# Optimization experiments

Measured on AMD Instinct MI355X. Metric: run time of the kernel, lower is better.

The kernel has to match this reference:

```python
import jax, jax.numpy as jnp
import numpy as np

DIM = 1024
NUM_HEADS = 16
HEAD_DIM = DIM // NUM_HEADS
B, S = 2, 2048


def setup_inputs() -> dict:
    key = jax.random.key(0)
    ks = jax.random.split(key, 7)
    x = jax.random.normal(ks[0], (B, S, DIM), dtype=jnp.float32)
    cos = jax.random.uniform(ks[1], (S, HEAD_DIM // 2), dtype=jnp.float32)
    sin = jax.random.uniform(ks[2], (S, HEAD_DIM // 2), dtype=jnp.float32)
    scale = 1.0 / np.sqrt(DIM)
    Wq = jax.random.normal(ks[3], (DIM, DIM), dtype=jnp.float32) * scale
    Wk = jax.random.normal(ks[4], (DIM, DIM), dtype=jnp.float32) * scale
    Wv = jax.random.normal(ks[5], (DIM, DIM), dtype=jnp.float32) * scale
    Wo = jax.random.normal(ks[6], (DIM, DIM), dtype=jnp.float32) * scale
    return {"x": x, "cos": cos, "sin": sin, "Wq": Wq, "Wk": Wk, "Wv": Wv, "Wo": Wo}


def _apply_rope(t, c, s):
    # t: [B, S, H, hd]; c, s: [1, S, 1, hd] (already doubled)
    half = t.shape[-1] // 2
    t1, t2 = t[..., :half], t[..., half:]
    rot = jnp.concatenate([-t2, t1], axis=-1)
    return t * c + rot * s


def reference(x, cos, sin, Wq, Wk, Wv, Wo):
    Bs, Ss, D = x.shape
    H, hd = NUM_HEADS, HEAD_DIM
    q = (x @ Wq).reshape(Bs, Ss, H, hd)
    k = (x @ Wk).reshape(Bs, Ss, H, hd)
    v = (x @ Wv).reshape(Bs, Ss, H, hd)
    # repeat(1,1,1,2) in torch tiles cos as [cos, cos] along last dim
    c = jnp.concatenate([cos, cos], axis=-1)[None, :, None, :]
    s = jnp.concatenate([sin, sin], axis=-1)[None, :, None, :]
    q = _apply_rope(q, c, s)
    k = _apply_rope(k, c, s)
    # SDPA, non-causal, scale 1/sqrt(hd)
    scores = jnp.einsum("bqhd,bkhd->bhqk", q, k) / jnp.sqrt(jnp.float32(hd))
    attn = jax.nn.softmax(scores, axis=-1)
    out = jnp.einsum("bhqk,bkhd->bqhd", attn, v).reshape(Bs, Ss, D)
    return out @ Wo
```

## Files before the change

### kernel.cpp

```cpp
#include <hip/hip_runtime.h>

#define B_  2
#define S_  2048
#define D_  1024
#define H_  16
#define HD_ 64
#define M_  (B_*S_)

typedef __bf16 bf16x8 __attribute__((ext_vector_type(8)));
typedef float  f32x4  __attribute__((ext_vector_type(4)));
typedef float  f32x16 __attribute__((ext_vector_type(16)));
typedef unsigned short ushort_t;

static __device__ __forceinline__ ushort_t f2bf(float f) {
  __bf16 b = (__bf16)f;
  return __builtin_bit_cast(ushort_t, b);
}
static __device__ __forceinline__ float bf2f(ushort_t u) {
  return (float)__builtin_bit_cast(__bf16, u);
}

__global__ __launch_bounds__(256) void convert_x(const float* __restrict__ x,
                                                 ushort_t* __restrict__ xb) {
  size_t e = ((size_t)blockIdx.x * 256 + threadIdx.x) * 8;
  float4 a = *(const float4*)(x + e);
  float4 b = *(const float4*)(x + e + 4);
  uint4 pk;
  pk.x = (unsigned)f2bf(a.x) | ((unsigned)f2bf(a.y) << 16);
  pk.y = (unsigned)f2bf(a.z) | ((unsigned)f2bf(a.w) << 16);
  pk.z = (unsigned)f2bf(b.x) | ((unsigned)f2bf(b.y) << 16);
  pk.w = (unsigned)f2bf(b.z) | ((unsigned)f2bf(b.w) << 16);
  *(uint4*)(xb + e) = pk;
}

__global__ __launch_bounds__(256) void transpose_w(const float* __restrict__ Wq,
                                                   const float* __restrict__ Wk,
                                                   const float* __restrict__ Wv,
                                                   const float* __restrict__ Wo,
                                                   ushort_t* __restrict__ Wqkvt,
                                                   ushort_t* __restrict__ Wot) {
  __shared__ __bf16 T[64][72];
  const int z = blockIdx.z;
  const float* W = (z == 0) ? Wq : (z == 1) ? Wk : (z == 2) ? Wv : Wo;
  ushort_t* Wt = (z < 3) ? (Wqkvt + (size_t)z * 1048576) : Wot;
  const int k0 = blockIdx.y * 64, n0 = blockIdx.x * 64;
  const int t = threadIdx.x, r = t >> 2, c16 = (t & 3) * 16;
#pragma unroll
  for (int i = 0; i < 4; i++) {
    float4 v = *(const float4*)(W + (size_t)(k0 + r) * D_ + n0 + c16 + i * 4);
    T[r][c16 + i*4 + 0] = (__bf16)v.x;
    T[r][c16 + i*4 + 1] = (__bf16)v.y;
    T[r][c16 + i*4 + 2] = (__bf16)v.z;
    T[r][c16 + i*4 + 3] = (__bf16)v.w;
  }
  __syncthreads();
  ushort_t vals[16];
#pragma unroll
  for (int i = 0; i < 16; i++) vals[i] = __builtin_bit_cast(ushort_t, T[c16 + i][r]);
  ushort_t* dst = Wt + (size_t)(n0 + r) * D_ + k0 + c16;
  *(uint4*)dst       = *(const uint4*)&vals[0];
  *(uint4*)(dst + 8) = *(const uint4*)&vals[8];
}

template<int OMODE>
__global__ __launch_bounds__(256) void gemm_bf16(const ushort_t* __restrict__ A,
                                                 const ushort_t* __restrict__ Bt,
                                                 void* __restrict__ Cp) {
  __shared__ __bf16 As[128][40];
  __shared__ __bf16 Bs[128][40];
  const int t = threadIdx.x, w = t >> 6, lane = t & 63, l15 = lane & 15, g = lane >> 4;
  const int wr = w >> 1, wc = w & 1;
  const int row0 = blockIdx.y * 128, col0 = blockIdx.x * 128;
  const int rr = t >> 2, c8 = (t & 3) * 8;
  f32x4 acc[4][4] = {};

  for (int k0 = 0; k0 < D_; k0 += 32) {
    __syncthreads();
#pragma unroll
    for (int p = 0; p < 2; p++) {
      uint4 va = *(const uint4*)(A  + (size_t)(row0 + p*64 + rr) * D_ + k0 + c8);
      *(uint4*)&As[p*64 + rr][c8] = va;
      uint4 vb = *(const uint4*)(Bt + (size_t)(col0 + p*64 + rr) * D_ + k0 + c8);
      *(uint4*)&Bs[p*64 + rr][c8] = vb;
    }
    __syncthreads();
    bf16x8 af[4], bfv[4];
#pragma unroll
    for (int mt = 0; mt < 4; mt++) af[mt]  = *(const bf16x8*)&As[wr*64 + mt*16 + l15][g*8];
#pragma unroll
    for (int nt = 0; nt < 4; nt++) bfv[nt] = *(const bf16x8*)&Bs[wc*64 + nt*16 + l15][g*8];
#pragma unroll
    for (int mt = 0; mt < 4; mt++)
#pragma unroll
      for (int nt = 0; nt < 4; nt++)
        acc[mt][nt] = __builtin_amdgcn_mfma_f32_16x16x32_bf16(af[mt], bfv[nt], acc[mt][nt], 0, 0, 0);
  }

#pragma unroll
  for (int mt = 0; mt < 4; mt++) {
#pragma unroll
    for (int nt = 0; nt < 4; nt++) {
      int col = col0 + wc*64 + nt*16 + l15;
#pragma unroll
      for (int reg = 0; reg < 4; reg++) {
        int r = row0 + wr*64 + mt*16 + g*4 + reg;
        float v = acc[mt][nt][reg];
        if (OMODE == 0) {
          ((float*)Cp)[(size_t)r * D_ + col] = v;
        } else {
          int mat = col >> 10, nc = col & 1023;
          int h = nc >> 6, d = nc & 63;
          int b = r >> 11, s = r & (S_ - 1);
          ((ushort_t*)Cp)[(size_t)mat * 4194304 +
                          (((size_t)(b*H_ + h) * S_ + s) << 6) + d] = f2bf(v);
        }
      }
    }
  }
}

__global__ __launch_bounds__(256) void rope_qk_bf(ushort_t* __restrict__ Q,
                                                  ushort_t* __restrict__ Kt,
                                                  const float* __restrict__ cosb,
                                                  const float* __restrict__ sinb) {
  int idx = blockIdx.x * 256 + threadIdx.x;
  int d = idx & 31, s = (idx >> 5) & (S_-1), bh = idx >> 16;
  size_t base = ((size_t)bh * S_ + s) * HD_;
  const float QS = 0.125f * 1.4426950408889634f;
  float c = cosb[s*32 + d], sn = sinb[s*32 + d];
  float q1 = bf2f(Q[base+d]), q2 = bf2f(Q[base+d+32]);
  Q[base+d]    = f2bf((q1*c - q2*sn) * QS);
  Q[base+d+32] = f2bf((q2*c + q1*sn) * QS);
  float k1 = bf2f(Kt[base+d]), k2 = bf2f(Kt[base+d+32]);
  Kt[base+d]    = f2bf(k1*c - k2*sn);
  Kt[base+d+32] = f2bf(k2*c + k1*sn);
}

__global__ __launch_bounds__(256) void attn32(const ushort_t* __restrict__ Q,
                                              const ushort_t* __restrict__ K,
                                              const ushort_t* __restrict__ V,
                                              ushort_t* __restrict__ Oa) {
  __shared__ __bf16 Ks[64][72];
  __shared__ __bf16 Vt[64][72];
  __shared__ __bf16 Ps[4][32][72];
  const int t = threadIdx.x, w = t >> 6, lane = t & 63;
  const int l31 = lane & 31, h2 = lane >> 5;
  const int bh = blockIdx.y, q0 = blockIdx.x * 128 + w * 32;

  const ushort_t* Qp = Q + ((size_t)bh * S_ + q0 + l31) * HD_;
  bf16x8 qf[4];
#pragma unroll
  for (int kc = 0; kc < 4; kc++) qf[kc] = *(const bf16x8*)(Qp + kc*16 + h2*8);

  f32x16 o0 = {}, o1 = {};
  float lp[16];
#pragma unroll
  for (int i = 0; i < 16; i++) lp[i] = 0.f;

  const ushort_t* Kb = K + (size_t)bh * S_ * HD_;
  const ushort_t* Vb = V + (size_t)bh * S_ * HD_;

  for (int kt = 0; kt < S_ / 64; kt++) {
    __syncthreads();
    {
      int r = t >> 3, d8 = (t & 7) * 8;
#pragma unroll
      for (int p = 0; p < 2; p++) {
        int key = r + p*32;
        uint4 v = *(const uint4*)(Kb + (size_t)(kt*64 + key) * HD_ + d8);
        *(uint4*)&Ks[key][d8] = v;
      }
    }
    {
      int kp = t & 31, db = (t >> 5) * 8;
      const ushort_t* vp = Vb + (size_t)(kt*64 + 2*kp) * HD_ + db;
      uint4 a = *(const uint4*)vp;
      uint4 b = *(const uint4*)(vp + HD_);
      const ushort_t* as = (const ushort_t*)&a;
      const ushort_t* bs = (const ushort_t*)&b;
#pragma unroll
      for (int j = 0; j < 8; j++)
        *(unsigned*)&Vt[db + j][2*kp] = (unsigned)as[j] | ((unsigned)bs[j] << 16);
    }
    __syncthreads();

    f32x16 s0 = {}, s1 = {};
#pragma unroll
    for (int kc = 0; kc < 4; kc++) {
      bf16x8 b0 = *(const bf16x8*)&Ks[l31][kc*16 + h2*8];
      bf16x8 b1 = *(const bf16x8*)&Ks[32 + l31][kc*16 + h2*8];
      s0 = __builtin_amdgcn_mfma_f32_32x32x16_bf16(qf[kc], b0, s0, 0, 0, 0);
      s1 = __builtin_amdgcn_mfma_f32_32x32x16_bf16(qf[kc], b1, s1, 0, 0, 0);
    }

#pragma unroll
    for (int i = 0; i < 16; i++) {
      float p0 = exp2f(s0[i]);
      float p1 = exp2f(s1[i]);
      lp[i] += p0 + p1;
      int row = (i & 3) + 8*(i >> 2) + 4*h2;
      Ps[w][row][l31]      = (__bf16)p0;
      Ps[w][row][32 + l31] = (__bf16)p1;
    }

#pragma unroll
    for (int kc = 0; kc < 4; kc++) {
      bf16x8 pf = *(const bf16x8*)&Ps[w][l31][kc*16 + h2*8];
      bf16x8 v0 = *(const bf16x8*)&Vt[l31][kc*16 + h2*8];
      bf16x8 v1 = *(const bf16x8*)&Vt[32 + l31][kc*16 + h2*8];
      o0 = __builtin_amdgcn_mfma_f32_32x32x16_bf16(pf, v0, o0, 0, 0, 0);
      o1 = __builtin_amdgcn_mfma_f32_32x32x16_bf16(pf, v1, o1, 0, 0, 0);
    }
  }

#pragma unroll
  for (int i = 0; i < 16; i++) {
#pragma unroll
    for (int mk = 1; mk < 32; mk <<= 1) lp[i] += __shfl_xor(lp[i], mk, 64);
  }

  int b = bh >> 4, h = bh & 15;
#pragma unroll
  for (int i = 0; i < 16; i++) {
    float inv = 1.f / lp[i];
    int row = q0 + (i & 3) + 8*(i >> 2) + 4*h2;
    size_t base = (size_t)(b*S_ + row) * D_ + h*64;
    Oa[base + l31]      = f2bf(o0[i] * inv);
    Oa[base + 32 + l31] = f2bf(o1[i] * inv);
  }
}

extern "C" void kernel_launch(void* const* d_in, const int* in_sizes, int n_in,
                              void* d_out, int out_size, void* d_ws, size_t ws_size,
                              hipStream_t stream) {
  (void)in_sizes; (void)n_in; (void)out_size; (void)ws_size;
  const float* x    = (const float*)d_in[0];
  const float* cosb = (const float*)d_in[1];
  const float* sinb = (const float*)d_in[2];
  const float* Wq   = (const float*)d_in[3];
  const float* Wk   = (const float*)d_in[4];
  const float* Wv   = (const float*)d_in[5];
  const float* Wo   = (const float*)d_in[6];
  float* out = (float*)d_out;

  ushort_t* w     = (ushort_t*)d_ws;
  ushort_t* xb    = w;
  ushort_t* Wqkvt = w + 4194304;
  ushort_t* Wot   = w + 7340032;
  ushort_t* Qb    = w + 8388608;
  ushort_t* Kb    = w + 12582912;
  ushort_t* Vb    = w + 16777216;
  ushort_t* att   = w + 20971520;

  convert_x<<<2048, 256, 0, stream>>>(x, xb);
  transpose_w<<<dim3(16, 16, 4), 256, 0, stream>>>(Wq, Wk, Wv, Wo, Wqkvt, Wot);

  gemm_bf16<1><<<dim3(24, 32), 256, 0, stream>>>(xb, Wqkvt, Qb);

  rope_qk_bf<<<8192, 256, 0, stream>>>(Qb, Kb, cosb, sinb);

  attn32<<<dim3(16, 32), 256, 0, stream>>>(Qb, Kb, Vb, att);

  gemm_bf16<0><<<dim3(8, 32), 256, 0, stream>>>(att, Wot, out);
}
```

Baseline: 241.9 us.

## Fuse RoPE into QKV GEMM, pre-transpose V, prefetch attention tiles, use LDS DMA

The RoPE and Q-scaling pass moves into the QKV GEMM epilogue, which removes a separate read-modify-write pass over Q and K. V gets its own transpose kernel, with a permutation that matches the packed P layout, so the attention loop no longer transposes V in shared memory. The next K/V tile is register-prefetched to overlap the loads with compute. The GEMM loads use global_load_lds with an unpadded LDS layout, which may cause bank conflicts on the fragment reads, and P is stored as packed pairs.

```diff
diff --git a/kernel.cpp b/kernel.cpp
--- a/kernel.cpp
+++ b/kernel.cpp
@@ -16,8 +16,11 @@
   __bf16 b = (__bf16)f;
   return __builtin_bit_cast(ushort_t, b);
 }
-static __device__ __forceinline__ float bf2f(ushort_t u) {
-  return (float)__builtin_bit_cast(__bf16, u);
+
+typedef __attribute__((address_space(1))) const unsigned u32g;
+typedef __attribute__((address_space(3))) unsigned u32l;
+static __device__ __forceinline__ void gll16(const ushort_t* g, __bf16* l) {
+  __builtin_amdgcn_global_load_lds((u32g*)g, (u32l*)l, 16, 0, 0);
 }
 
 __global__ __launch_bounds__(256) void convert_x(const float* __restrict__ x,
@@ -62,33 +65,54 @@
   *(uint4*)(dst + 8) = *(const uint4*)&vals[8];
 }
 
+__global__ __launch_bounds__(256) void transpose_v(const ushort_t* __restrict__ Vb,
+                                                   ushort_t* __restrict__ Vtg) {
+  __shared__ __bf16 T[64][72];
+  const int bh = blockIdx.y, kt = blockIdx.x;
+  const int t = threadIdx.x, r = t >> 2, c16 = (t & 3) * 16;
+  const ushort_t* src = Vb + ((size_t)bh * S_ + kt*64 + r) * 64 + c16;
+  *(uint4*)&T[r][c16]     = *(const uint4*)src;
+  *(uint4*)&T[r][c16 + 8] = *(const uint4*)(src + 8);
+  __syncthreads();
+  ushort_t vals[16];
+#pragma unroll
+  for (int i = 0; i < 16; i++) {
+    int c = c16 + i;
+    int k = ((c & 1) << 5) | (c >> 1);
+    vals[i] = __builtin_bit_cast(ushort_t, T[k][r]);
+  }
+  ushort_t* dst = Vtg + ((size_t)bh * 64 + r) * S_ + kt*64 + c16;
+  *(uint4*)dst       = *(const uint4*)&vals[0];
+  *(uint4*)(dst + 8) = *(const uint4*)&vals[8];
+}
+
 template<int OMODE>
 __global__ __launch_bounds__(256) void gemm_bf16(const ushort_t* __restrict__ A,
                                                  const ushort_t* __restrict__ Bt,
-                                                 void* __restrict__ Cp) {
-  __shared__ __bf16 As[128][40];
-  __shared__ __bf16 Bs[128][40];
+                                                 void* __restrict__ Cp,
+                                                 const float* __restrict__ cosb,
+                                                 const float* __restrict__ sinb) {
+  __shared__ __bf16 As[4096];
+  __shared__ __bf16 Bs[4096];
   const int t = threadIdx.x, w = t >> 6, lane = t & 63, l15 = lane & 15, g = lane >> 4;
   const int wr = w >> 1, wc = w & 1;
   const int row0 = blockIdx.y * 128, col0 = blockIdx.x * 128;
-  const int rr = t >> 2, c8 = (t & 3) * 8;
+  const int lr = t >> 2, lc = (t & 3) * 8;
   f32x4 acc[4][4] = {};
 
   for (int k0 = 0; k0 < D_; k0 += 32) {
     __syncthreads();
 #pragma unroll
-    for (int p = 0; p < 2; p++) {
-      uint4 va = *(const uint4*)(A  + (size_t)(row0 + p*64 + rr) * D_ + k0 + c8);
-      *(uint4*)&As[p*64 + rr][c8] = va;
-      uint4 vb = *(const uint4*)(Bt + (size_t)(col0 + p*64 + rr) * D_ + k0 + c8);
-      *(uint4*)&Bs[p*64 + rr][c8] = vb;
+    for (int i = 0; i < 2; i++) {
+      gll16(A  + (size_t)(row0 + i*64 + lr) * D_ + k0 + lc, &As[i*2048 + w*512]);
+      gll16(Bt + (size_t)(col0 + i*64 + lr) * D_ + k0 + lc, &Bs[i*2048 + w*512]);
     }
     __syncthreads();
     bf16x8 af[4], bfv[4];
 #pragma unroll
-    for (int mt = 0; mt < 4; mt++) af[mt]  = *(const bf16x8*)&As[wr*64 + mt*16 + l15][g*8];
-#pragma unroll
-    for (int nt = 0; nt < 4; nt++) bfv[nt] = *(const bf16x8*)&Bs[wc*64 + nt*16 + l15][g*8];
+    for (int mt = 0; mt < 4; mt++) af[mt]  = *(const bf16x8*)&As[(wr*64 + mt*16 + l15)*32 + g*8];
+#pragma unroll
+    for (int nt = 0; nt < 4; nt++) bfv[nt] = *(const bf16x8*)&Bs[(wc*64 + nt*16 + l15)*32 + g*8];
 #pragma unroll
     for (int mt = 0; mt < 4; mt++)
 #pragma unroll
@@ -96,49 +120,57 @@
         acc[mt][nt] = __builtin_amdgcn_mfma_f32_16x16x32_bf16(af[mt], bfv[nt], acc[mt][nt], 0, 0, 0);
   }
 
-#pragma unroll
-  for (int mt = 0; mt < 4; mt++) {
-#pragma unroll
-    for (int nt = 0; nt < 4; nt++) {
-      int col = col0 + wc*64 + nt*16 + l15;
+  if (OMODE == 0) {
+#pragma unroll
+    for (int mt = 0; mt < 4; mt++)
+#pragma unroll
+      for (int nt = 0; nt < 4; nt++) {
+        int col = col0 + wc*64 + nt*16 + l15;
+#pragma unroll
+        for (int reg = 0; reg < 4; reg++) {
+          int r = row0 + wr*64 + mt*16 + g*4 + reg;
+          ((float*)Cp)[(size_t)r * D_ + col] = acc[mt][nt][reg];
+        }
+      }
+  } else {
+    const int mat = col0 >> 10;
+    const int nc0 = (col0 + wc*64) & 1023;
+    const int h = nc0 >> 6;
+    ushort_t* dst = (ushort_t*)Cp + (size_t)mat * 4194304;
+    const float QS = 0.125f * 1.4426950408889634f;
+#pragma unroll
+    for (int mt = 0; mt < 4; mt++) {
 #pragma unroll
       for (int reg = 0; reg < 4; reg++) {
         int r = row0 + wr*64 + mt*16 + g*4 + reg;
-        float v = acc[mt][nt][reg];
-        if (OMODE == 0) {
-          ((float*)Cp)[(size_t)r * D_ + col] = v;
+        int b = r >> 11, s = r & (S_ - 1);
+        size_t base = (((size_t)(b*H_ + h) * S_ + s) << 6);
+        if (mat < 2) {
+#pragma unroll
+          for (int nt = 0; nt < 2; nt++) {
+            int d1 = nt*16 + l15;
+            float c  = cosb[s*32 + d1];
+            float sn = sinb[s*32 + d1];
+            float v1 = acc[mt][nt][reg], v2 = acc[mt][nt+2][reg];
+            float r1 = v1*c - v2*sn;
+            float r2 = v2*c + v1*sn;
+            if (mat == 0) { r1 *= QS; r2 *= QS; }
+            dst[base + d1]      = f2bf(r1);
+            dst[base + d1 + 32] = f2bf(r2);
+          }
         } else {
-          int mat = col >> 10, nc = col & 1023;
-          int h = nc >> 6, d = nc & 63;
-          int b = r >> 11, s = r & (S_ - 1);
-          ((ushort_t*)Cp)[(size_t)mat * 4194304 +
-                          (((size_t)(b*H_ + h) * S_ + s) << 6) + d] = f2bf(v);
+#pragma unroll
+          for (int nt = 0; nt < 4; nt++)
+            dst[base + nt*16 + l15] = f2bf(acc[mt][nt][reg]);
         }
       }
     }
   }
 }
 
-__global__ __launch_bounds__(256) void rope_qk_bf(ushort_t* __restrict__ Q,
-                                                  ushort_t* __restrict__ Kt,
-                                                  const float* __restrict__ cosb,
-                                                  const float* __restrict__ sinb) {
-  int idx = blockIdx.x * 256 + threadIdx.x;
-  int d = idx & 31, s = (idx >> 5) & (S_-1), bh = idx >> 16;
-  size_t base = ((size_t)bh * S_ + s) * HD_;
-  const float QS = 0.125f * 1.4426950408889634f;
-  float c = cosb[s*32 + d], sn = sinb[s*32 + d];
-  float q1 = bf2f(Q[base+d]), q2 = bf2f(Q[base+d+32]);
-  Q[base+d]    = f2bf((q1*c - q2*sn) * QS);
-  Q[base+d+32] = f2bf((q2*c + q1*sn) * QS);
-  float k1 = bf2f(Kt[base+d]), k2 = bf2f(Kt[base+d+32]);
-  Kt[base+d]    = f2bf(k1*c - k2*sn);
-  Kt[base+d+32] = f2bf(k2*c + k1*sn);
-}
-
 __global__ __launch_bounds__(256) void attn32(const ushort_t* __restrict__ Q,
                                               const ushort_t* __restrict__ K,
-                                              const ushort_t* __restrict__ V,
+                                              const ushort_t* __restrict__ Vtg,
                                               ushort_t* __restrict__ Oa) {
   __shared__ __bf16 Ks[64][72];
   __shared__ __bf16 Vt[64][72];
@@ -157,32 +189,31 @@
 #pragma unroll
   for (int i = 0; i < 16; i++) lp[i] = 0.f;
 
-  const ushort_t* Kb = K + (size_t)bh * S_ * HD_;
-  const ushort_t* Vb = V + (size_t)bh * S_ * HD_;
+  const ushort_t* Kb = K   + (size_t)bh * S_ * HD_;
+  const ushort_t* Vg = Vtg + (size_t)bh * HD_ * S_;
+  const int sr = t >> 3, sc8 = (t & 7) * 8;
+
+  uint4 ka, kb, va, vb;
+  {
+    ka = *(const uint4*)(Kb + (size_t)(sr)      * HD_ + sc8);
+    kb = *(const uint4*)(Kb + (size_t)(sr + 32) * HD_ + sc8);
+    va = *(const uint4*)(Vg + (size_t)(sr)      * S_  + sc8);
+    vb = *(const uint4*)(Vg + (size_t)(sr + 32) * S_  + sc8);
+  }
 
   for (int kt = 0; kt < S_ / 64; kt++) {
     __syncthreads();
-    {
-      int r = t >> 3, d8 = (t & 7) * 8;
-#pragma unroll
-      for (int p = 0; p < 2; p++) {
-        int key = r + p*32;
-        uint4 v = *(const uint4*)(Kb + (size_t)(kt*64 + key) * HD_ + d8);
-        *(uint4*)&Ks[key][d8] = v;
-      }
-    }
-    {
-      int kp = t & 31, db = (t >> 5) * 8;
-      const ushort_t* vp = Vb + (size_t)(kt*64 + 2*kp) * HD_ + db;
-      uint4 a = *(const uint4*)vp;
-      uint4 b = *(const uint4*)(vp + HD_);
-      const ushort_t* as = (const ushort_t*)&a;
-      const ushort_t* bs = (const ushort_t*)&b;
-#pragma unroll
-      for (int j = 0; j < 8; j++)
-        *(unsigned*)&Vt[db + j][2*kp] = (unsigned)as[j] | ((unsigned)bs[j] << 16);
-    }
-    __syncthreads();
+    *(uint4*)&Ks[sr][sc8]      = ka;
+    *(uint4*)&Ks[sr + 32][sc8] = kb;
+    *(uint4*)&Vt[sr][sc8]      = va;
+    *(uint4*)&Vt[sr + 32][sc8] = vb;
+    __syncthreads();
+    if (kt < S_/64 - 1) {
+      ka = *(const uint4*)(Kb + (size_t)((kt+1)*64 + sr)      * HD_ + sc8);
+      kb = *(const uint4*)(Kb + (size_t)((kt+1)*64 + sr + 32) * HD_ + sc8);
+      va = *(const uint4*)(Vg + (size_t)(sr)      * S_ + (kt+1)*64 + sc8);
+      vb = *(const uint4*)(Vg + (size_t)(sr + 32) * S_ + (kt+1)*64 + sc8);
+    }
 
     f32x16 s0 = {}, s1 = {};
 #pragma unroll
@@ -199,8 +230,8 @@
       float p1 = exp2f(s1[i]);
       lp[i] += p0 + p1;
       int row = (i & 3) + 8*(i >> 2) + 4*h2;
-      Ps[w][row][l31]      = (__bf16)p0;
-      Ps[w][row][32 + l31] = (__bf16)p1;
+      unsigned pk = (unsigned)f2bf(p0) | ((unsigned)f2bf(p1) << 16);
+      *(unsigned*)&Ps[w][row][2*l31] = pk;
     }
 
 #pragma unroll
@@ -250,16 +281,17 @@
   ushort_t* Qb    = w + 8388608;
   ushort_t* Kb    = w + 12582912;
   ushort_t* Vb    = w + 16777216;
-  ushort_t* att   = w + 20971520;
+  ushort_t* Vtg   = w + 20971520;
+  ushort_t* att   = w + 25165824;
 
   convert_x<<<2048, 256, 0, stream>>>(x, xb);
   transpose_w<<<dim3(16, 16, 4), 256, 0, stream>>>(Wq, Wk, Wv, Wo, Wqkvt, Wot);
 
-  gemm_bf16<1><<<dim3(24, 32), 256, 0, stream>>>(xb, Wqkvt, Qb);
-
-  rope_qk_bf<<<8192, 256, 0, stream>>>(Qb, Kb, cosb, sinb);
-
-  attn32<<<dim3(16, 32), 256, 0, stream>>>(Qb, Kb, Vb, att);
-
-  gemm_bf16<0><<<dim3(8, 32), 256, 0, stream>>>(att, Wot, out);
-}
+  gemm_bf16<1><<<dim3(24, 32), 256, 0, stream>>>(xb, Wqkvt, Qb, cosb, sinb);
+
+  transpose_v<<<dim3(32, 32), 256, 0, stream>>>(Vb, Vtg);
+
+  attn32<<<dim3(16, 32), 256, 0, stream>>>(Qb, Kb, Vtg, att);
+
+  gemm_bf16<0><<<dim3(8, 32), 256, 0, stream>>>(att, Wot, out, nullptr, nullptr);
+}
```

Result: faster. 224.4 us (-7.2%).
